# Optimization experiments

Hardware: AMD Instinct MI355X
Metric: run time of the kernel (lower is better)

## Reference

```python
import jax, jax.numpy as jnp
import numpy as np

EPS = 1e-5

def sage_conv(x, edge_index, w_l, b_l, w_r):
    # PyG SAGEConv with mean aggregation: lin_l(mean of source-neighbor feats per dst) + lin_r(x)
    n = x.shape[0]
    src, dst = edge_index[0], edge_index[1]
    agg = jax.ops.segment_sum(x[src], dst, num_segments=n)  # [N, d]
    deg = jax.ops.segment_sum(jnp.ones((edge_index.shape[1],), x.dtype), dst, num_segments=n)
    agg = agg / jnp.maximum(deg, 1.0)[:, None]
    return agg @ w_l + b_l + x @ w_r

def batchnorm_eval(x, gamma, beta, mean, var):
    return (x - mean) * (gamma * jax.lax.rsqrt(var + EPS)) + beta

def setup_inputs() -> dict:
    key = jax.random.key(0)
    ks = jax.random.split(key, 12)
    N, E, D, H, O = 10000, 160000, 512, 512, 256
    inp = {
        'x': jax.random.normal(ks[0], (N, D), jnp.float32),
        'edge_index': jax.random.randint(ks[1], (2, E), 0, N, jnp.int32),
        'w_l1': jax.random.normal(ks[2], (D, H), jnp.float32) * (1.0 / np.sqrt(D)),
        'b1': jnp.zeros((H,), jnp.float32),
        'w_r1': jax.random.normal(ks[3], (D, H), jnp.float32) * (1.0 / np.sqrt(D)),
        'bn1_gamma': jnp.ones((H,), jnp.float32),
        'bn1_beta': jnp.zeros((H,), jnp.float32),
        'bn1_mean': jax.random.normal(ks[4], (H,), jnp.float32) * 0.1,
        'bn1_var': jax.random.uniform(ks[5], (H,), jnp.float32, 0.5, 1.5),
        'w_l2': jax.random.normal(ks[6], (H, H), jnp.float32) * (1.0 / np.sqrt(H)),
        'b2': jnp.zeros((H,), jnp.float32),
        'w_r2': jax.random.normal(ks[7], (H, H), jnp.float32) * (1.0 / np.sqrt(H)),
        'bn2_gamma': jnp.ones((H,), jnp.float32),
        'bn2_beta': jnp.zeros((H,), jnp.float32),
        'bn2_mean': jax.random.normal(ks[8], (H,), jnp.float32) * 0.1,
        'bn2_var': jax.random.uniform(ks[9], (H,), jnp.float32, 0.5, 1.5),
        'w_l3': jax.random.normal(ks[10], (H, O), jnp.float32) * (1.0 / np.sqrt(H)),
        'b3': jnp.zeros((O,), jnp.float32),
        'w_r3': jax.random.normal(ks[11], (H, O), jnp.float32) * (1.0 / np.sqrt(H)),
    }
    return inp

def reference(x, edge_index, w_l1, b1, w_r1, bn1_gamma, bn1_beta, bn1_mean, bn1_var,
              w_l2, b2, w_r2, bn2_gamma, bn2_beta, bn2_mean, bn2_var,
              w_l3, b3, w_r3):
    # Layer 1: SAGEConv -> BN (eval) -> ReLU (dropout is identity in eval)
    h = sage_conv(x, edge_index, w_l1, b1, w_r1)
    h = jax.nn.relu(batchnorm_eval(h, bn1_gamma, bn1_beta, bn1_mean, bn1_var))
    # Layer 2
    h = sage_conv(h, edge_index, w_l2, b2, w_r2)
    h = jax.nn.relu(batchnorm_eval(h, bn2_gamma, bn2_beta, bn2_mean, bn2_var))
    # Layer 3 (no BN/ReLU)
    return sage_conv(h, edge_index, w_l3, b3, w_r3)
```

## Files before the change

### kernel.cpp

```cpp
#include <hip/hip_runtime.h>

#define NNODE 10000
#define NEDGE 160000

using frag8 = __attribute__((ext_vector_type(8))) short;
using f32x4 = __attribute__((ext_vector_type(4))) float;

__device__ __forceinline__ unsigned short f2bf(float f) {
    union { float f; unsigned u; } v; v.f = f;
    unsigned r = (v.u + 0x7fffu + ((v.u >> 16) & 1u)) >> 16;
    return (unsigned short)r;
}
__device__ __forceinline__ float bf2f(unsigned short s) {
    union { unsigned u; float f; } v; v.u = ((unsigned)s) << 16; return v.f;
}

__global__ __launch_bounds__(1024) void k_scan(const int* __restrict__ deg,
                                               int* __restrict__ rs,
                                               int* __restrict__ cur, int n, int total) {
    const int tid = threadIdx.x;
    const int CH = 10;
    const int base = tid * CH;
    int vals[CH];
    int tsum = 0;
#pragma unroll
    for (int j = 0; j < CH; j++) {
        int v = (base + j < n) ? deg[base + j] : 0;
        vals[j] = v; tsum += v;
    }
    const int lane = tid & 63, wid = tid >> 6;
    int x = tsum;
#pragma unroll
    for (int d = 1; d < 64; d <<= 1) {
        int y = __shfl_up(x, d, 64);
        if (lane >= d) x += y;
    }
    __shared__ int wt[16];
    if (lane == 63) wt[wid] = x;
    __syncthreads();
    if (tid == 0) {
        int c = 0;
#pragma unroll
        for (int k = 0; k < 16; k++) { int t = wt[k]; wt[k] = c; c += t; }
    }
    __syncthreads();
    int run = wt[wid] + x - tsum;
#pragma unroll
    for (int j = 0; j < CH; j++) {
        if (base + j < n) { rs[base + j] = run; cur[base + j] = run; }
        run += vals[j];
    }
    if (tid == 0) rs[n] = total;
}

__global__ void k_fill(const int* __restrict__ src, const int* __restrict__ dst,
                       int E, int* __restrict__ cur, int* __restrict__ csr) {
    int e = blockIdx.x * 256 + threadIdx.x;
    if (e < E) {
        int p = atomicAdd(&cur[dst[e]], 1);
        csr[p] = src[e];
    }
}

__global__ __launch_bounds__(256) void k_prep(
    const float* __restrict__ x, unsigned short* __restrict__ xb,
    const float* __restrict__ wl1, const float* __restrict__ wr1,
    const float* __restrict__ wl2, const float* __restrict__ wr2,
    const float* __restrict__ wl3, const float* __restrict__ wr3,
    unsigned short* __restrict__ bt1, unsigned short* __restrict__ bt2,
    unsigned short* __restrict__ bt3,
    const float* __restrict__ b1, const float* __restrict__ g1, const float* __restrict__ be1,
    const float* __restrict__ m1, const float* __restrict__ v1,
    const float* __restrict__ b2, const float* __restrict__ g2, const float* __restrict__ be2,
    const float* __restrict__ m2, const float* __restrict__ v2,
    const float* __restrict__ b3,
    float* __restrict__ sc1, float* __restrict__ sh1,
    float* __restrict__ sc2, float* __restrict__ sh2,
    float* __restrict__ sc3, float* __restrict__ sh3,
    const int* __restrict__ dstI, int* __restrict__ deg) {
    const int b = blockIdx.x, tid = threadIdx.x;
    if (b < 5000) {
        int i = b * 256 + tid;
        float4 f = ((const float4*)x)[i];
        ushort4 o;
        o.x = f2bf(f.x); o.y = f2bf(f.y); o.z = f2bf(f.z); o.w = f2bf(f.w);
        ((ushort4*)xb)[i] = o;
        return;
    }
    if (b >= 6281) {
        int e = (b - 6281) * 256 + tid;
        if (e < NEDGE) atomicAdd(&deg[dstI[e]], 1);
        return;
    }
    if (b == 6280) {
        for (int t = tid; t < 512; t += 256) {
            float s1 = g1[t] * rsqrtf(v1[t] + 1e-5f);
            sc1[t] = s1; sh1[t] = (b1[t] - m1[t]) * s1 + be1[t];
            float s2 = g2[t] * rsqrtf(v2[t] + 1e-5f);
            sc2[t] = s2; sh2[t] = (b2[t] - m2[t]) * s2 + be2[t];
        }
        if (tid < 256) { sc3[tid] = 1.0f; sh3[tid] = b3[tid]; }
        return;
    }
    __shared__ float t[32][33];
    int tj = b - 5000;
    const float* srcp; unsigned short* dstp; int C, koff, ntilesN;
    if (tj < 1024) {
        int job = tj >> 8; int tile = tj & 255; C = 512; ntilesN = 16;
        srcp = (job == 0) ? wl1 : (job == 1) ? wr1 : (job == 2) ? wl2 : wr2;
        dstp = (job < 2) ? bt1 : bt2; koff = (job & 1) * 512;
        tj = tile;
    } else {
        int jj = tj - 1024; int job = jj >> 7; int tile = jj & 127; C = 256; ntilesN = 8;
        srcp = (job == 0) ? wl3 : wr3; dstp = bt3; koff = job * 512;
        tj = tile;
    }
    int k0 = (tj / ntilesN) * 32, c0 = (tj % ntilesN) * 32;
    int tx = tid & 31, ty = tid >> 5;
#pragma unroll
    for (int q = 0; q < 4; q++)
        t[ty + 8 * q][tx] = srcp[(long)(k0 + ty + 8 * q) * C + c0 + tx];
    __syncthreads();
#pragma unroll
    for (int q = 0; q < 4; q++)
        dstp[(long)(c0 + ty + 8 * q) * 1024 + koff + k0 + tx] = f2bf(t[tx][ty + 8 * q]);
}

__global__ __launch_bounds__(64) void k_agg(const unsigned short* __restrict__ S,
                                            const int* __restrict__ rs, const int* __restrict__ csr,
                                            unsigned short* __restrict__ outb) {
    const int n = blockIdx.x;
    const int c = blockIdx.y * 128 + threadIdx.x * 2;
    const int s = rs[n], e = rs[n + 1];
    float a0 = 0.f, a1 = 0.f;
    int i = s;
    for (; i + 4 <= e; i += 4) {
        int r0 = csr[i], r1 = csr[i + 1], r2 = csr[i + 2], r3 = csr[i + 3];
        unsigned u0 = *(const unsigned*)(S + (long)r0 * 512 + c);
        unsigned u1 = *(const unsigned*)(S + (long)r1 * 512 + c);
        unsigned u2 = *(const unsigned*)(S + (long)r2 * 512 + c);
        unsigned u3 = *(const unsigned*)(S + (long)r3 * 512 + c);
        a0 += bf2f((unsigned short)(u0 & 0xffffu)); a1 += bf2f((unsigned short)(u0 >> 16));
        a0 += bf2f((unsigned short)(u1 & 0xffffu)); a1 += bf2f((unsigned short)(u1 >> 16));
        a0 += bf2f((unsigned short)(u2 & 0xffffu)); a1 += bf2f((unsigned short)(u2 >> 16));
        a0 += bf2f((unsigned short)(u3 & 0xffffu)); a1 += bf2f((unsigned short)(u3 >> 16));
    }
    for (; i < e; i++) {
        unsigned u = *(const unsigned*)(S + (long)csr[i] * 512 + c);
        a0 += bf2f((unsigned short)(u & 0xffffu)); a1 += bf2f((unsigned short)(u >> 16));
    }
    const int cnt = e - s;
    const float inv = 1.f / (float)(cnt > 1 ? cnt : 1);
    unsigned o = (unsigned)f2bf(a0 * inv) | ((unsigned)f2bf(a1 * inv) << 16);
    *(unsigned*)(outb + (long)n * 512 + c) = o;
}

template <int MODE, int NOUT>
__global__ __launch_bounds__(256) void k_gemm(const unsigned short* __restrict__ Agg,
                                              const unsigned short* __restrict__ Self,
                                              const unsigned short* __restrict__ Bt,
                                              const float* __restrict__ sc, const float* __restrict__ sh,
                                              unsigned short* __restrict__ hout, float* __restrict__ fout,
                                              int M) {
    constexpr int NT = NOUT / 64;
    constexpr int QSH = (NT == 8) ? 6 : 5;
    const int b = blockIdx.x;
    const int X = b & 7;
    const int q = (b >> 3) & (NT - 1);
    const int g = b >> QSH;
    const int mstrip = g * 8 + X;
    const int m0 = mstrip * 128;
    if (m0 >= M) return;
    const int n0 = q * 64;

    __shared__ __align__(16) short As[2][128 * 64];
    __shared__ __align__(16) short Bs[2][64 * 64];
    const int tid = threadIdx.x;
    const int w = tid >> 6, lane = tid & 63;
    const int wm = (w >> 1) * 64, wn = (w & 1) * 32;
    const int fr = lane & 15;
    const int fq = lane >> 4;
    const int sw = fr & 7;

    const int srow = w * 8 + (lane >> 3);
    const int scol = (((lane & 7) ^ (lane >> 3)) * 8);
    const int ldsOff = w * 8 * 64;

    f32x4 acc[4][2];
#pragma unroll
    for (int i = 0; i < 4; i++)
#pragma unroll
        for (int j = 0; j < 2; j++)
#pragma unroll
            for (int r = 0; r < 4; r++) acc[i][j][r] = 0.f;

    auto issue = [&](int t, int buf) {
        const short* abase = (const short*)((t < 8) ? Agg : Self);
        const int kk = (t & 7) * 64;
        const int k0 = t * 64;
#pragma unroll
        for (int cch = 0; cch < 4; cch++)
            __builtin_amdgcn_global_load_lds(
                (const __attribute__((address_space(1))) void*)(abase + (long)(m0 + cch * 32 + srow) * 512 + kk + scol),
                (__attribute__((address_space(3))) void*)(&As[buf][ldsOff + cch * 32 * 64]), 16, 0, 0);
#pragma unroll
        for (int cch = 0; cch < 2; cch++)
            __builtin_amdgcn_global_load_lds(
                (const __attribute__((address_space(1))) void*)((const short*)Bt + (long)(n0 + cch * 32 + srow) * 1024 + k0 + scol),
                (__attribute__((address_space(3))) void*)(&Bs[buf][ldsOff + cch * 32 * 64]), 16, 0, 0);
    };

    issue(0, 0);
#pragma unroll
    for (int t = 0; t < 16; t++) {
        const int cur = t & 1;
        __syncthreads();
        if (t < 15) issue(t + 1, cur ^ 1);
#pragma unroll
        for (int ks = 0; ks < 2; ks++) {
            frag8 af[4], bf[2];
#pragma unroll
            for (int i = 0; i < 4; i++)
                af[i] = *(const frag8*)(&As[cur][(wm + i * 16 + fr) * 64 + (((ks * 4 + fq) ^ sw) * 8)]);
#pragma unroll
            for (int j = 0; j < 2; j++)
                bf[j] = *(const frag8*)(&Bs[cur][(wn + j * 16 + fr) * 64 + (((ks * 4 + fq) ^ sw) * 8)]);
#pragma unroll
            for (int i = 0; i < 4; i++)
#pragma unroll
                for (int j = 0; j < 2; j++)
                    acc[i][j] = __builtin_amdgcn_mfma_f32_16x16x32_bf16(af[i], bf[j], acc[i][j], 0, 0, 0);
        }
        __syncthreads();
    }

    float scj[2], shj[2];
#pragma unroll
    for (int j = 0; j < 2; j++) {
        int col = n0 + wn + j * 16 + fr;
        scj[j] = sc[col]; shj[j] = sh[col];
    }
#pragma unroll
    for (int i = 0; i < 4; i++) {
        int rowb = m0 + wm + i * 16 + fq * 4;
#pragma unroll
        for (int j = 0; j < 2; j++) {
            int col = n0 + wn + j * 16 + fr;
#pragma unroll
            for (int r = 0; r < 4; r++) {
                int row = rowb + r;
                if (row < M) {
                    float y = acc[i][j][r] * scj[j] + shj[j];
                    if constexpr (MODE == 0) {
                        y = fmaxf(y, 0.f);
                        hout[(long)row * 512 + col] = f2bf(y);
                    } else {
                        fout[(long)row * NOUT + col] = y;
                    }
                }
            }
        }
    }
}

extern "C" void kernel_launch(void* const* d_in, const int* in_sizes, int n_in,
                              void* d_out, int out_size, void* d_ws, size_t ws_size,
                              hipStream_t stream) {
    const float* x    = (const float*)d_in[0];
    const int*   ei   = (const int*)d_in[1];
    const float* w_l1 = (const float*)d_in[2];
    const float* b1   = (const float*)d_in[3];
    const float* w_r1 = (const float*)d_in[4];
    const float* g1   = (const float*)d_in[5];
    const float* be1  = (const float*)d_in[6];
    const float* m1   = (const float*)d_in[7];
    const float* v1   = (const float*)d_in[8];
    const float* w_l2 = (const float*)d_in[9];
    const float* b2   = (const float*)d_in[10];
    const float* w_r2 = (const float*)d_in[11];
    const float* g2   = (const float*)d_in[12];
    const float* be2  = (const float*)d_in[13];
    const float* m2   = (const float*)d_in[14];
    const float* v2   = (const float*)d_in[15];
    const float* w_l3 = (const float*)d_in[16];
    const float* b3   = (const float*)d_in[17];
    const float* w_r3 = (const float*)d_in[18];
    float* out = (float*)d_out;

    const int N = NNODE, E = NEDGE;
    const int* srcI = ei;
    const int* dstI = ei + E;

    char* w = (char*)d_ws;
    auto alloc = [&](size_t bytes) { void* p = (void*)w; w += (bytes + 255) & ~(size_t)255; return p; };
    int* deg = (int*)alloc((size_t)N * 4);
    int* rs  = (int*)alloc((size_t)(N + 1) * 4);
    int* cur = (int*)alloc((size_t)N * 4);
    int* csr = (int*)alloc((size_t)E * 4);
    unsigned short* xb   = (unsigned short*)alloc((size_t)N * 512 * 2);
    unsigned short* bt1  = (unsigned short*)alloc((size_t)512 * 1024 * 2);
    unsigned short* bt2  = (unsigned short*)alloc((size_t)512 * 1024 * 2);
    unsigned short* bt3  = (unsigned short*)alloc((size_t)256 * 1024 * 2);
    float* sc1 = (float*)alloc(512 * 4); float* sh1 = (float*)alloc(512 * 4);
    float* sc2 = (float*)alloc(512 * 4); float* sh2 = (float*)alloc(512 * 4);
    float* sc3 = (float*)alloc(256 * 4); float* sh3 = (float*)alloc(256 * 4);
    unsigned short* agg_a = (unsigned short*)alloc((size_t)N * 512 * 2);
    unsigned short* h1    = (unsigned short*)alloc((size_t)N * 512 * 2);
    unsigned short* h2    = (unsigned short*)alloc((size_t)N * 512 * 2);
    (void)alloc(256 * 1024);

    hipMemsetAsync(deg, 0, (size_t)N * 4, stream);
    k_prep<<<6906, 256, 0, stream>>>(x, xb, w_l1, w_r1, w_l2, w_r2, w_l3, w_r3,
                                     bt1, bt2, bt3,
                                     b1, g1, be1, m1, v1, b2, g2, be2, m2, v2, b3,
                                     sc1, sh1, sc2, sh2, sc3, sh3, dstI, deg);
    k_scan<<<1, 1024, 0, stream>>>(deg, rs, cur, N, E);
    k_fill<<<(E + 255) / 256, 256, 0, stream>>>(srcI, dstI, E, cur, csr);

    dim3 ga(N, 4);

    k_agg<<<ga, 64, 0, stream>>>(xb, rs, csr, agg_a);
    k_gemm<0, 512><<<640, 256, 0, stream>>>(agg_a, xb, bt1, sc1, sh1, h1, nullptr, N);
    k_agg<<<ga, 64, 0, stream>>>(h1, rs, csr, agg_a);
    k_gemm<0, 512><<<640, 256, 0, stream>>>(agg_a, h1, bt2, sc2, sh2, h2, nullptr, N);
    k_agg<<<ga, 64, 0, stream>>>(h2, rs, csr, agg_a);
    k_gemm<1, 256><<<320, 256, 0, stream>>>(agg_a, h2, bt3, sc3, sh3, nullptr, out, N);
}
```

Measured before the change: 251.8 us.

## Load GEMM A fragments directly from global and widen aggregation loads

The GEMM kernel no longer stages the A tile (aggregated and self features) through LDS. Each wave reads its A MFMA fragments straight from global memory, while B keeps LDS double buffering. This removes one barrier per k-step and adds an occupancy hint of 4 blocks per SM. The aggregation kernel now has each thread gather 4 bf16 values with 8-byte loads, which halves the grid's y dimension. The trade-off is less coalesced, L2-dependent global reads for A, and A data is no longer shared between waves through LDS.

Result: slower. 327.7 us (+30.2%).

```diff
diff --git a/kernel.cpp b/kernel.cpp
--- a/kernel.cpp
+++ b/kernel.cpp
@@ -130,62 +130,69 @@
                                             const int* __restrict__ rs, const int* __restrict__ csr,
                                             unsigned short* __restrict__ outb) {
     const int n = blockIdx.x;
-    const int c = blockIdx.y * 128 + threadIdx.x * 2;
+    const int c = blockIdx.y * 256 + threadIdx.x * 4;
     const int s = rs[n], e = rs[n + 1];
-    float a0 = 0.f, a1 = 0.f;
+    float a0 = 0.f, a1 = 0.f, a2 = 0.f, a3 = 0.f;
     int i = s;
     for (; i + 4 <= e; i += 4) {
         int r0 = csr[i], r1 = csr[i + 1], r2 = csr[i + 2], r3 = csr[i + 3];
-        unsigned u0 = *(const unsigned*)(S + (long)r0 * 512 + c);
-        unsigned u1 = *(const unsigned*)(S + (long)r1 * 512 + c);
-        unsigned u2 = *(const unsigned*)(S + (long)r2 * 512 + c);
-        unsigned u3 = *(const unsigned*)(S + (long)r3 * 512 + c);
-        a0 += bf2f((unsigned short)(u0 & 0xffffu)); a1 += bf2f((unsigned short)(u0 >> 16));
-        a0 += bf2f((unsigned short)(u1 & 0xffffu)); a1 += bf2f((unsigned short)(u1 >> 16));
-        a0 += bf2f((unsigned short)(u2 & 0xffffu)); a1 += bf2f((unsigned short)(u2 >> 16));
-        a0 += bf2f((unsigned short)(u3 & 0xffffu)); a1 += bf2f((unsigned short)(u3 >> 16));
+        uint2 u0 = *(const uint2*)(S + (long)r0 * 512 + c);
+        uint2 u1 = *(const uint2*)(S + (long)r1 * 512 + c);
+        uint2 u2 = *(const uint2*)(S + (long)r2 * 512 + c);
+        uint2 u3 = *(const uint2*)(S + (long)r3 * 512 + c);
+        a0 += bf2f((unsigned short)(u0.x & 0xffffu)); a1 += bf2f((unsigned short)(u0.x >> 16));
+        a2 += bf2f((unsigned short)(u0.y & 0xffffu)); a3 += bf2f((unsigned short)(u0.y >> 16));
+        a0 += bf2f((unsigned short)(u1.x & 0xffffu)); a1 += bf2f((unsigned short)(u1.x >> 16));
+        a2 += bf2f((unsigned short)(u1.y & 0xffffu)); a3 += bf2f((unsigned short)(u1.y >> 16));
+        a0 += bf2f((unsigned short)(u2.x & 0xffffu)); a1 += bf2f((unsigned short)(u2.x >> 16));
+        a2 += bf2f((unsigned short)(u2.y & 0xffffu)); a3 += bf2f((unsigned short)(u2.y >> 16));
+        a0 += bf2f((unsigned short)(u3.x & 0xffffu)); a1 += bf2f((unsigned short)(u3.x >> 16));
+        a2 += bf2f((unsigned short)(u3.y & 0xffffu)); a3 += bf2f((unsigned short)(u3.y >> 16));
     }
     for (; i < e; i++) {
-        unsigned u = *(const unsigned*)(S + (long)csr[i] * 512 + c);
-        a0 += bf2f((unsigned short)(u & 0xffffu)); a1 += bf2f((unsigned short)(u >> 16));
+        uint2 u = *(const uint2*)(S + (long)csr[i] * 512 + c);
+        a0 += bf2f((unsigned short)(u.x & 0xffffu)); a1 += bf2f((unsigned short)(u.x >> 16));
+        a2 += bf2f((unsigned short)(u.y & 0xffffu)); a3 += bf2f((unsigned short)(u.y >> 16));
     }
     const int cnt = e - s;
     const float inv = 1.f / (float)(cnt > 1 ? cnt : 1);
-    unsigned o = (unsigned)f2bf(a0 * inv) | ((unsigned)f2bf(a1 * inv) << 16);
-    *(unsigned*)(outb + (long)n * 512 + c) = o;
+    uint2 o;
+    o.x = (unsigned)f2bf(a0 * inv) | ((unsigned)f2bf(a1 * inv) << 16);
+    o.y = (unsigned)f2bf(a2 * inv) | ((unsigned)f2bf(a3 * inv) << 16);
+    *(uint2*)(outb + (long)n * 512 + c) = o;
 }
 
 template <int MODE, int NOUT>
-__global__ __launch_bounds__(256) void k_gemm(const unsigned short* __restrict__ Agg,
-                                              const unsigned short* __restrict__ Self,
-                                              const unsigned short* __restrict__ Bt,
-                                              const float* __restrict__ sc, const float* __restrict__ sh,
-                                              unsigned short* __restrict__ hout, float* __restrict__ fout,
-                                              int M) {
+__global__ __launch_bounds__(256, 4) void k_gemm(const unsigned short* __restrict__ Agg,
+                                                 const unsigned short* __restrict__ Self,
+                                                 const unsigned short* __restrict__ Bt,
+                                                 const float* __restrict__ sc, const float* __restrict__ sh,
+                                                 unsigned short* __restrict__ hout, float* __restrict__ fout,
+                                                 int M) {
     constexpr int NT = NOUT / 64;
     constexpr int QSH = (NT == 8) ? 6 : 5;
     const int b = blockIdx.x;
     const int X = b & 7;
     const int q = (b >> 3) & (NT - 1);
     const int g = b >> QSH;
-    const int mstrip = g * 8 + X;
-    const int m0 = mstrip * 128;
+    const int m0 = (g * 8 + X) * 128;
     if (m0 >= M) return;
     const int n0 = q * 64;
 
-    __shared__ __align__(16) short As[2][128 * 64];
     __shared__ __align__(16) short Bs[2][64 * 64];
     const int tid = threadIdx.x;
     const int w = tid >> 6, lane = tid & 63;
     const int wm = (w >> 1) * 64, wn = (w & 1) * 32;
-    const int fr = lane & 15;
-    const int fq = lane >> 4;
-    const int sw = fr & 7;
-
+    const int fr = lane & 15, fq = lane >> 4, sw = fr & 7;
     const int srow = w * 8 + (lane >> 3);
     const int scol = (((lane & 7) ^ (lane >> 3)) * 8);
     const int ldsOff = w * 8 * 64;
 
+    long aoff[4];
+#pragma unroll
+    for (int i = 0; i < 4; i++)
+        aoff[i] = (long)(m0 + wm + i * 16 + fr) * 512 + fq * 8;
+
     f32x4 acc[4][2];
 #pragma unroll
     for (int i = 0; i < 4; i++)
@@ -194,15 +201,8 @@
 #pragma unroll
             for (int r = 0; r < 4; r++) acc[i][j][r] = 0.f;
 
-    auto issue = [&](int t, int buf) {
-        const short* abase = (const short*)((t < 8) ? Agg : Self);
-        const int kk = (t & 7) * 64;
+    auto issueB = [&](int t, int buf) {
         const int k0 = t * 64;
-#pragma unroll
-        for (int cch = 0; cch < 4; cch++)
-            __builtin_amdgcn_global_load_lds(
-                (const __attribute__((address_space(1))) void*)(abase + (long)(m0 + cch * 32 + srow) * 512 + kk + scol),
-                (__attribute__((address_space(3))) void*)(&As[buf][ldsOff + cch * 32 * 64]), 16, 0, 0);
 #pragma unroll
         for (int cch = 0; cch < 2; cch++)
             __builtin_amdgcn_global_load_lds(
@@ -210,18 +210,23 @@
                 (__attribute__((address_space(3))) void*)(&Bs[buf][ldsOff + cch * 32 * 64]), 16, 0, 0);
     };
 
-    issue(0, 0);
+    issueB(0, 0);
 #pragma unroll
     for (int t = 0; t < 16; t++) {
         const int cur = t & 1;
+        const short* abase = (const short*)((t < 8) ? Agg : Self);
+        const int kk = (t & 7) * 64;
         __syncthreads();
-        if (t < 15) issue(t + 1, cur ^ 1);
+        if (t < 15) issueB(t + 1, cur ^ 1);
+        frag8 af[2][4];
+#pragma unroll
+        for (int ks = 0; ks < 2; ks++)
+#pragma unroll
+            for (int i = 0; i < 4; i++)
+                af[ks][i] = *(const frag8*)(abase + aoff[i] + kk + ks * 32);
 #pragma unroll
         for (int ks = 0; ks < 2; ks++) {
-            frag8 af[4], bf[2];
-#pragma unroll
-            for (int i = 0; i < 4; i++)
-                af[i] = *(const frag8*)(&As[cur][(wm + i * 16 + fr) * 64 + (((ks * 4 + fq) ^ sw) * 8)]);
+            frag8 bf[2];
 #pragma unroll
             for (int j = 0; j < 2; j++)
                 bf[j] = *(const frag8*)(&Bs[cur][(wn + j * 16 + fr) * 64 + (((ks * 4 + fq) ^ sw) * 8)]);
@@ -229,9 +234,8 @@
             for (int i = 0; i < 4; i++)
 #pragma unroll
                 for (int j = 0; j < 2; j++)
-                    acc[i][j] = __builtin_amdgcn_mfma_f32_16x16x32_bf16(af[i], bf[j], acc[i][j], 0, 0, 0);
+                    acc[i][j] = __builtin_amdgcn_mfma_f32_16x16x32_bf16(af[ks][i], bf[j], acc[i][j], 0, 0, 0);
         }
-        __syncthreads();
     }
 
     float scj[2], shj[2];
@@ -317,7 +321,7 @@
     k_scan<<<1, 1024, 0, stream>>>(deg, rs, cur, N, E);
     k_fill<<<(E + 255) / 256, 256, 0, stream>>>(srcI, dstI, E, cur, csr);
 
-    dim3 ga(N, 4);
+    dim3 ga(N, 2);
 
     k_agg<<<ga, 64, 0, stream>>>(xb, rs, csr, agg_a);
     k_gemm<0, 512><<<640, 256, 0, stream>>>(agg_a, xb, bt1, sc1, sh1, h1, nullptr, N);
```
